# Kernel optimization log

Hardware: AMD Instinct MI355X
Metric: run time of the kernel (lower is better)

## Reference

```python
import jax, jax.numpy as jnp
import numpy as np
import math

B, S, HID, H, DH = 4, 1024, 1024, 16, 64  # batch, seq, hidden, heads, head_dim


def _rotate_half(x):
    x1, x2 = jnp.split(x, 2, axis=-1)
    return jnp.concatenate([-x2, x1], axis=-1)


def _apply_rope(t, freqs):
    # t: [B,H,S,DH], freqs: [S,rot_dim]; here rot_dim == DH so no pass-through part
    rot = freqs.shape[-1]
    cos_ = jnp.cos(freqs)[None, None, :, :].astype(t.dtype)
    sin_ = jnp.sin(freqs)[None, None, :, :].astype(t.dtype)
    t_rot, t_pass = t[..., :rot], t[..., rot:]
    t_rot = t_rot * cos_ + _rotate_half(t_rot) * sin_
    return jnp.concatenate([t_rot, t_pass], axis=-1)


def setup_inputs() -> dict:
    key = jax.random.key(0)
    ks = jax.random.split(key, 8)
    hidden_states = jax.random.normal(ks[0], (B, S, HID), dtype=jnp.float32)
    # additive mask: valid prefix of random length per batch row, -1e9 on padding
    lengths = jax.random.randint(ks[1], (B,), 3 * S // 4, S + 1)
    pos = jnp.arange(S)
    attention_mask = jnp.where(pos[None, :] < lengths[:, None], 0.0, -1e9)
    attention_mask = attention_mask.astype(jnp.float32)[:, None, None, :]  # [B,1,1,S]
    # rotary frequencies: standard RoPE angles, duplicated halves -> [S, DH]
    inv_freq = 1.0 / (10000.0 ** (jnp.arange(0, DH // 2, dtype=jnp.float32) / (DH // 2)))
    ang = pos.astype(jnp.float32)[:, None] * inv_freq[None, :]
    freqs = jnp.concatenate([ang, ang], axis=-1)  # [S, DH]
    sc = 0.02
    Wq = jax.random.normal(ks[2], (HID, HID), dtype=jnp.float32) * sc
    Wk = jax.random.normal(ks[3], (HID, HID), dtype=jnp.float32) * sc
    Wv = jax.random.normal(ks[4], (HID, HID), dtype=jnp.float32) * sc
    bq = jnp.zeros((HID,), dtype=jnp.float32)
    bk = jnp.zeros((HID,), dtype=jnp.float32)
    bv = jnp.zeros((HID,), dtype=jnp.float32)
    return dict(hidden_states=hidden_states, attention_mask=attention_mask, freqs=freqs,
                Wq=Wq, bq=bq, Wk=Wk, bk=bk, Wv=Wv, bv=bv)


def reference(hidden_states, attention_mask, freqs, Wq, bq, Wk, bk, Wv, bv):
    b, s, _ = hidden_states.shape
    # QKV projections -> [B,H,S,DH]
    q = (hidden_states @ Wq + bq).reshape(b, s, H, DH).transpose(0, 2, 1, 3)
    k = (hidden_states @ Wk + bk).reshape(b, s, H, DH).transpose(0, 2, 1, 3)
    v = (hidden_states @ Wv + bv).reshape(b, s, H, DH).transpose(0, 2, 1, 3)
    # inline RoPE on q and k (same freqs for both, as (rotary_pos_emb,)*2)
    q = _apply_rope(q, freqs)
    k = _apply_rope(k, freqs)
    scores = jnp.einsum('bhqd,bhkd->bhqk', q, k) / math.sqrt(DH)
    scores = scores + attention_mask  # additive mask broadcast over [B,H,S,S]
    probs = jax.nn.softmax(scores, axis=-1)
    # no_prob_mask filtering: zero out masked key columns
    probs = jnp.where(attention_mask < -1e-5, 0.0, probs)
    # dropout prob is 0.0 (eval) -> identity
    ctx = jnp.einsum('bhqk,bhkd->bhqd', probs, v)
    ctx = ctx.transpose(0, 2, 1, 3).reshape(b, s, H * DH)
    return ctx
```

## Files before the change

kernel.cpp:

```cpp
#include <hip/hip_runtime.h>
#include <hip/hip_bf16.h>
#include <cmath>

#define NB   4
#define NS   1024
#define NHID 1024
#define NH   16
#define NDH  64
#define QKV_PLANE (NB * NH * NS * NDH)

typedef __attribute__((ext_vector_type(8))) short bf16x8;
typedef __attribute__((ext_vector_type(4))) float f32x4;
typedef __attribute__((ext_vector_type(8))) unsigned short u16x8;

typedef __attribute__((address_space(1))) const void gv_t;
typedef __attribute__((address_space(3))) void       lv_t;

__device__ __forceinline__ void gload16(const void* g, void* l) {
    __builtin_amdgcn_global_load_lds((gv_t*)g, (lv_t*)l, 16, 0, 0);
}

__device__ __forceinline__ unsigned short f2b(float f) {
    union { float f; unsigned int u; } v; v.f = f;
    unsigned int r = (v.u + 0x7fff + ((v.u >> 16) & 1)) >> 16;
    return (unsigned short)r;
}

__device__ __forceinline__ unsigned int f2b2(float a, float b) {
    __hip_bfloat162 h = __float22bfloat162_rn(make_float2(a, b));
    union { __hip_bfloat162 h; unsigned int u; } v; v.h = h;
    return v.u;
}

__device__ __forceinline__ float fexp2(float x) {
#if __has_builtin(__builtin_amdgcn_exp2f)
    return __builtin_amdgcn_exp2f(x);
#else
    return exp2f(x);
#endif
}

__global__ __launch_bounds__(256) void prep_kernel(
    const float* __restrict__ hs, const float* __restrict__ freqs,
    const float* __restrict__ Wq, const float* __restrict__ Wk,
    const float* __restrict__ Wv,
    unsigned short* __restrict__ hsb, unsigned short* __restrict__ wt,
    float2* __restrict__ cs)
{
    const int z   = blockIdx.z;
    const int tid = threadIdx.x;

    if (z == 3) {
        const int bx = blockIdx.y * 16 + blockIdx.x;
        #pragma unroll
        for (int c = 0; c < 16; ++c) {
            const int idx = bx * 16384 + (c * 256 + tid) * 4;
            float4 v = *(const float4*)&hs[idx];
            ushort4 o;
            o.x = f2b(v.x); o.y = f2b(v.y); o.z = f2b(v.z); o.w = f2b(v.w);
            *(ushort4*)&hsb[idx] = o;
        }
        return;
    }
    if (z == 4) {
        const int bx = blockIdx.y * 16 + blockIdx.x;
        if (bx < 128) {
            const int id = bx * 256 + tid;
            const int s = id >> 5, d = id & 31;
            const float ang = freqs[s * NDH + d];
            float sn, cn;
            sincosf(ang, &sn, &cn);
            cs[id] = make_float2(cn, sn);
        }
        return;
    }

    const float* __restrict__ W = (z == 0) ? Wq : (z == 1) ? Wk : Wv;
    __shared__ float t[64][65];
    const int k0 = blockIdx.x * 64, n0 = blockIdx.y * 64;
    #pragma unroll
    for (int c = 0; c < 16; ++c) {
        const int flat = c * 256 + tid;
        const int r = flat >> 6, cc = flat & 63;
        t[r][cc] = W[(size_t)(k0 + r) * NHID + n0 + cc];
    }
    __syncthreads();
    #pragma unroll
    for (int c = 0; c < 16; ++c) {
        const int flat = c * 256 + tid;
        const int r = flat >> 6, cc = flat & 63;
        wt[(size_t)(z * 1024 + n0 + r) * NHID + k0 + cc] = f2b(t[cc][r]);
    }
}

__global__ __launch_bounds__(256) void fused_gemm_kernel(
    const unsigned short* __restrict__ hsb,
    const unsigned short* __restrict__ wt,
    const float2* __restrict__ cs,
    const float* __restrict__ bq, const float* __restrict__ bk,
    const float* __restrict__ bv,
    unsigned short* __restrict__ qkv)
{
    __shared__ short SH[16896];
    short* As = SH;
    short* Bs = SH + 8192;

    const int tid  = threadIdx.x;
    const int lane = tid & 63;
    const int wv   = __builtin_amdgcn_readfirstlane(tid >> 6);
    const bool vmode = (blockIdx.x >= 16);

    const unsigned short* Amat;
    const unsigned short* Bmat;
    int a_base, b_base, m0, n0, vb_ = 0;
    if (!vmode) {
        n0 = blockIdx.x * 128;
        m0 = blockIdx.y * 128;
        Amat = hsb;  a_base = m0;
        Bmat = wt;   b_base = n0;
    } else {
        m0  = (blockIdx.x - 16) * 128;
        vb_ = blockIdx.y >> 3;
        n0  = (blockIdx.y & 7) * 128;
        Amat = wt;   a_base = 2048 + m0;
        Bmat = hsb;  b_base = vb_ * 1024 + n0;
    }

    const int ri  = lane >> 3;
    const int kcs = ((lane & 7) ^ ri) * 8;
    const unsigned short* gA[4];
    const unsigned short* gB[4];
    short* lA[4];
    short* lB[4];
    #pragma unroll
    for (int j = 0; j < 4; ++j) {
        const int L = 4 * wv + j;
        gA[j] = Amat + (size_t)(a_base + L * 8 + ri) * NHID + kcs;
        gB[j] = Bmat + (size_t)(b_base + L * 8 + ri) * NHID + kcs;
        lA[j] = As + L * 512;
        lB[j] = Bs + L * 512;
    }

    const int R  = (wv & 1) * 64;
    const int CW = (wv >> 1) * 64;
    const int c0 = lane & 15;
    const int g  = lane >> 4;
    const int sw7 = c0 & 7;
    int aoff[4][2], boff[4][2];
    #pragma unroll
    for (int i = 0; i < 4; ++i)
        #pragma unroll
        for (int ks = 0; ks < 2; ++ks) {
            aoff[i][ks] = (R  + 16 * i + c0) * 64 + ((g + 4 * ks) ^ sw7) * 8;
            boff[i][ks] = (CW + 16 * i + c0) * 64 + ((g + 4 * ks) ^ sw7) * 8;
        }

    f32x4 acc[4][4] = {};

    for (int k0 = 0; k0 < NHID; k0 += 64) {
        __syncthreads();
        #pragma unroll
        for (int j = 0; j < 4; ++j) {
            gload16(gA[j] + k0, lA[j]);
            gload16(gB[j] + k0, lB[j]);
        }
        __syncthreads();
        #pragma unroll
        for (int ks = 0; ks < 2; ++ks) {
            bf16x8 af[4], bfr[4];
            #pragma unroll
            for (int i = 0; i < 4; ++i) af[i]  = *(const bf16x8*)&As[aoff[i][ks]];
            #pragma unroll
            for (int j = 0; j < 4; ++j) bfr[j] = *(const bf16x8*)&Bs[boff[j][ks]];
            #pragma unroll
            for (int i = 0; i < 4; ++i)
                #pragma unroll
                for (int j = 0; j < 4; ++j)
                    acc[i][j] = __builtin_amdgcn_mfma_f32_16x16x32_bf16(
                        af[i], bfr[j], acc[i][j], 0, 0, 0);
        }
    }

    __syncthreads();
    unsigned short* E = (unsigned short*)SH;
    const int qrow4 = (lane >> 4) * 4;

    if (!vmode) {
        const int z  = n0 >> 10;
        const int hd = ((n0 & 1023) + CW) >> 6;
        const float* __restrict__ bb = (z == 0) ? bq : bk;
        const float b0 = bb[hd * 64 + c0];
        const float b1 = bb[hd * 64 + c0 + 16];
        const float b2 = bb[hd * 64 + c0 + 32];
        const float b3 = bb[hd * 64 + c0 + 48];

        #pragma unroll
        for (int i = 0; i < 4; ++i) {
            #pragma unroll
            for (int r = 0; r < 4; ++r) {
                const int ml = R + qrow4 + 16 * i + r;
                const int s  = (m0 + ml) & 1023;
                float o0 = acc[i][0][r] + b0;
                float o1 = acc[i][1][r] + b1;
                float o2 = acc[i][2][r] + b2;
                float o3 = acc[i][3][r] + b3;
                const float2 cs0 = cs[s * 32 + c0];
                const float2 cs1 = cs[s * 32 + c0 + 16];
                unsigned short* e = E + ml * 132 + CW + c0;
                e[0]  = f2b(o0 * cs0.x - o2 * cs0.y);
                e[16] = f2b(o1 * cs1.x - o3 * cs1.y);
                e[32] = f2b(o2 * cs0.x + o0 * cs0.y);
                e[48] = f2b(o3 * cs1.x + o1 * cs1.y);
            }
        }
        __syncthreads();

        const int hd0 = (n0 & 1023) >> 6;
        unsigned short* __restrict__ base = qkv + (size_t)z * QKV_PLANE;
        #pragma unroll
        for (int c = 0; c < 8; ++c) {
            const int chunk = c * 256 + tid;
            const int row   = chunk >> 4;
            const int col16 = chunk & 15;
            const int m     = m0 + row;
            const int bidx  = m >> 10;
            const int s     = m & 1023;
            const int head  = hd0 + (col16 >> 3);
            const int d     = (col16 & 7) * 8;
            u16x8 v = *(const u16x8*)&E[row * 132 + col16 * 8];
            *(u16x8*)&base[(((size_t)bidx * NH + head) * NS + s) * NDH + d] = v;
        }
    } else {
        #pragma unroll
        for (int i = 0; i < 4; ++i) {
            #pragma unroll
            for (int r = 0; r < 4; ++r) {
                const int ml  = R + qrow4 + 16 * i + r;
                const float bvm = bv[m0 + ml];
                unsigned short* e = E + ml * 132 + CW + c0;
                e[0]  = f2b(acc[i][0][r] + bvm);
                e[16] = f2b(acc[i][1][r] + bvm);
                e[32] = f2b(acc[i][2][r] + bvm);
                e[48] = f2b(acc[i][3][r] + bvm);
            }
        }
        __syncthreads();

        unsigned short* __restrict__ vplane = qkv + 2 * (size_t)QKV_PLANE;
        #pragma unroll
        for (int c = 0; c < 8; ++c) {
            const int chunk = c * 256 + tid;
            const int row   = chunk >> 4;
            const int col16 = chunk & 15;
            u16x8 v = *(const u16x8*)&E[row * 132 + col16 * 8];
            *(u16x8*)&vplane[((size_t)(vb_ * 1024 + m0 + row)) * NS
                             + n0 + col16 * 8] = v;
        }
    }
}

__global__ __launch_bounds__(512) void attn_kernel(
    const unsigned short* __restrict__ qkv, const float* __restrict__ mask,
    float* __restrict__ out)
{
    const int qt = blockIdx.x, h = blockIdx.y, b = blockIdx.z;
    const unsigned short* qp  = qkv + ((size_t)(b * NH + h) * NS) * NDH;
    const unsigned short* kp  = qp + QKV_PLANE;
    const unsigned short* vtp = qkv + 2 * (size_t)QKV_PLANE
                              + ((size_t)(b * NH + h) * NDH) * NS;

    __shared__ unsigned short KsA[64 * 64];
    __shared__ unsigned short VtA[64 * 64];
    __shared__ unsigned short PsA[128 * 64];
    __shared__ float Mk[1024];
    __shared__ float Ll[128];

    const int tid  = threadIdx.x;
    const int lane = tid & 63;
    const int w    = __builtin_amdgcn_readfirstlane(tid >> 6);
    const int c0   = lane & 15;
    const int g    = lane >> 4;
    const int sw7  = c0 & 7;
    const float C1 = 0.125f * 1.44269504f;

    {
        const int i = tid * 2;
        float2 mv = *(const float2*)&mask[(size_t)b * NS + i];
        Mk[i]     = mv.x * 1.44269504f;
        Mk[i + 1] = mv.y * 1.44269504f;
    }

    bf16x8 qf[2];
    #pragma unroll
    for (int ks = 0; ks < 2; ++ks)
        qf[ks] = *(const bf16x8*)&qp[
            (size_t)(qt * 128 + w * 16 + c0) * NDH + g * 8 + ks * 32];

    const int i8 = lane >> 3, c8 = lane & 7;
    const int gsw = (c8 ^ i8) * 8;
    const unsigned short* gk = kp  + (size_t)(w * 8 + i8) * NDH + gsw;
    const unsigned short* gv = vtp + (size_t)(w * 8 + i8) * NS  + gsw;
    unsigned short* lk = KsA + w * 512;
    unsigned short* lv = VtA + w * 512;

    int kaddr[4][2], pw4[4], pr[2];
    #pragma unroll
    for (int mt = 0; mt < 4; ++mt)
        #pragma unroll
        for (int ks = 0; ks < 2; ++ks)
            kaddr[mt][ks] = (mt * 16 + c0) * 64 + ((g + ks * 4) ^ sw7) * 8;
    #pragma unroll
    for (int mt = 0; mt < 4; ++mt)
        pw4[mt] = (w * 16 + c0) * 64 + ((2 * mt + (g >> 1)) ^ sw7) * 8 + (g & 1) * 4;
    #pragma unroll
    for (int ks = 0; ks < 2; ++ks)
        pr[ks] = (w * 16 + c0) * 64 + ((g + ks * 4) ^ sw7) * 8;

    __syncthreads();
    int ktmax = 16;
    while (ktmax > 1 && Mk[(ktmax - 1) * 64] < -1.0f) --ktmax;

    float lrow = 0.f;
    f32x4 O[4] = {};

    for (int kt = 0; kt < ktmax; ++kt) {
        __syncthreads();
        gload16(gk, lk);
        gload16(gv, lv);
        gk += 64 * NDH;
        gv += 64;
        __syncthreads();

        bf16x8 kf[4][2];
        #pragma unroll
        for (int mt = 0; mt < 4; ++mt)
            #pragma unroll
            for (int ks = 0; ks < 2; ++ks)
                kf[mt][ks] = *(const bf16x8*)&KsA[kaddr[mt][ks]];
        f32x4 S[4];
        #pragma unroll
        for (int mt = 0; mt < 4; ++mt) {
            f32x4 a = {};
            a = __builtin_amdgcn_mfma_f32_16x16x32_bf16(kf[mt][0], qf[0], a, 0, 0, 0);
            a = __builtin_amdgcn_mfma_f32_16x16x32_bf16(kf[mt][1], qf[1], a, 0, 0, 0);
            S[mt] = a;
        }

        float psum = 0.f;
        #pragma unroll
        for (int mt = 0; mt < 4; ++mt) {
            float4 mv = *(const float4*)&Mk[kt * 64 + mt * 16 + g * 4];
            float p0 = fexp2(S[mt][0] * C1 + mv.x);
            float p1 = fexp2(S[mt][1] * C1 + mv.y);
            float p2 = fexp2(S[mt][2] * C1 + mv.z);
            float p3 = fexp2(S[mt][3] * C1 + mv.w);
            psum += (p0 + p1) + (p2 + p3);
            uint2 u;
            u.x = f2b2(p0, p1);
            u.y = f2b2(p2, p3);
            *(uint2*)&PsA[pw4[mt]] = u;
        }
        lrow += psum;

        bf16x8 pf[2], vf[4][2];
        #pragma unroll
        for (int ks = 0; ks < 2; ++ks)
            pf[ks] = *(const bf16x8*)&PsA[pr[ks]];
        #pragma unroll
        for (int nd = 0; nd < 4; ++nd)
            #pragma unroll
            for (int ks = 0; ks < 2; ++ks)
                vf[nd][ks] = *(const bf16x8*)&VtA[kaddr[nd][ks]];
        #pragma unroll
        for (int nd = 0; nd < 4; ++nd) {
            f32x4 o = O[nd];
            o = __builtin_amdgcn_mfma_f32_16x16x32_bf16(pf[0], vf[nd][0], o, 0, 0, 0);
            o = __builtin_amdgcn_mfma_f32_16x16x32_bf16(pf[1], vf[nd][1], o, 0, 0, 0);
            O[nd] = o;
        }
    }

    lrow += __shfl_xor(lrow, 16);
    lrow += __shfl_xor(lrow, 32);
    if (g == 0) Ll[w * 16 + c0] = lrow;
    float4 lv4 = *(const float4*)&Ll[w * 16 + g * 4];
    float inv[4];
    #pragma unroll
    for (int r = 0; r < 4; ++r) inv[r] = 1.0f / ((const float*)&lv4)[r];

    #pragma unroll
    for (int nd = 0; nd < 4; ++nd)
        #pragma unroll
        for (int r = 0; r < 4; ++r) {
            const int row = qt * 128 + w * 16 + g * 4 + r;
            const int col = h * 64 + nd * 16 + c0;
            out[((size_t)b * NS + row) * NHID + col] = O[nd][r] * inv[r];
        }
}

extern "C" void kernel_launch(void* const* d_in, const int* in_sizes, int n_in,
                              void* d_out, int out_size, void* d_ws, size_t ws_size,
                              hipStream_t stream) {
    const float* hs    = (const float*)d_in[0];
    const float* mask  = (const float*)d_in[1];
    const float* freqs = (const float*)d_in[2];
    const float* Wq    = (const float*)d_in[3];
    const float* bq    = (const float*)d_in[4];
    const float* Wk    = (const float*)d_in[5];
    const float* bk    = (const float*)d_in[6];
    const float* Wv    = (const float*)d_in[7];
    const float* bv    = (const float*)d_in[8];
    float* out = (float*)d_out;

    char* ws = (char*)d_ws;
    unsigned short* qkvb = (unsigned short*)ws;
    unsigned short* hsb  = (unsigned short*)(ws + 25165824);
    unsigned short* wtb  = (unsigned short*)(ws + 33554432);
    float2*         csb  = (float2*)       (ws + 39845888);

    prep_kernel<<<dim3(16, 16, 5), 256, 0, stream>>>(hs, freqs, Wq, Wk, Wv,
                                                     hsb, wtb, csb);
    fused_gemm_kernel<<<dim3(24, 32), 256, 0, stream>>>(hsb, wtb, csb,
                                                        bq, bk, bv, qkvb);
    attn_kernel<<<dim3(NS / 128, NH, NB), 512, 0, stream>>>(qkvb, mask, out);
}
```

Baseline: 155.7 us.

## Double-buffer K/V tiles in attention loop and raise MFMA wave priority

The attention kernel now keeps two LDS buffers for K and V^T. It prefetches the next 64-key tile with global_load_lds while the current tile is computed, which cuts the per-iteration barriers from two to one. The MFMA sections are wrapped in s_setprio to favour matrix issue across waves. LDS use grows by 16 KB per block, which may reduce occupancy. Correctness depends on the end-of-loop barrier waiting for the async LDS loads to finish.

```diff
diff --git a/kernel.cpp b/kernel.cpp
--- a/kernel.cpp
+++ b/kernel.cpp
@@ -269,8 +269,8 @@
     const unsigned short* vtp = qkv + 2 * (size_t)QKV_PLANE
                               + ((size_t)(b * NH + h) * NDH) * NS;
 
-    __shared__ unsigned short KsA[64 * 64];
-    __shared__ unsigned short VtA[64 * 64];
+    __shared__ unsigned short KsA[2][64 * 64];
+    __shared__ unsigned short VtA[2][64 * 64];
     __shared__ unsigned short PsA[128 * 64];
     __shared__ float Mk[1024];
     __shared__ float Ll[128];
@@ -298,10 +298,8 @@
 
     const int i8 = lane >> 3, c8 = lane & 7;
     const int gsw = (c8 ^ i8) * 8;
-    const unsigned short* gk = kp  + (size_t)(w * 8 + i8) * NDH + gsw;
-    const unsigned short* gv = vtp + (size_t)(w * 8 + i8) * NS  + gsw;
-    unsigned short* lk = KsA + w * 512;
-    unsigned short* lv = VtA + w * 512;
+    const unsigned short* gk0 = kp  + (size_t)(w * 8 + i8) * NDH + gsw;
+    const unsigned short* gv0 = vtp + (size_t)(w * 8 + i8) * NS  + gsw;
 
     int kaddr[4][2], pw4[4], pr[2];
     #pragma unroll
@@ -316,7 +314,10 @@
     for (int ks = 0; ks < 2; ++ks)
         pr[ks] = (w * 16 + c0) * 64 + ((g + ks * 4) ^ sw7) * 8;
 
+    gload16(gk0, &KsA[0][w * 512]);
+    gload16(gv0, &VtA[0][w * 512]);
     __syncthreads();
+
     int ktmax = 16;
     while (ktmax > 1 && Mk[(ktmax - 1) * 64] < -1.0f) --ktmax;
 
@@ -324,20 +325,24 @@
     f32x4 O[4] = {};
 
     for (int kt = 0; kt < ktmax; ++kt) {
-        __syncthreads();
-        gload16(gk, lk);
-        gload16(gv, lv);
-        gk += 64 * NDH;
-        gv += 64;
-        __syncthreads();
+        const int cur = kt & 1;
+
+        if (kt + 1 < ktmax) {
+            gload16(gk0 + (size_t)(kt + 1) * 64 * NDH, &KsA[cur ^ 1][w * 512]);
+            gload16(gv0 + (size_t)(kt + 1) * 64,       &VtA[cur ^ 1][w * 512]);
+        }
+
+        const unsigned short* Kb = KsA[cur];
+        const unsigned short* Vb = VtA[cur];
 
         bf16x8 kf[4][2];
         #pragma unroll
         for (int mt = 0; mt < 4; ++mt)
             #pragma unroll
             for (int ks = 0; ks < 2; ++ks)
-                kf[mt][ks] = *(const bf16x8*)&KsA[kaddr[mt][ks]];
+                kf[mt][ks] = *(const bf16x8*)&Kb[kaddr[mt][ks]];
         f32x4 S[4];
+        __builtin_amdgcn_s_setprio(1);
         #pragma unroll
         for (int mt = 0; mt < 4; ++mt) {
             f32x4 a = {};
@@ -345,6 +350,7 @@
             a = __builtin_amdgcn_mfma_f32_16x16x32_bf16(kf[mt][1], qf[1], a, 0, 0, 0);
             S[mt] = a;
         }
+        __builtin_amdgcn_s_setprio(0);
 
         float psum = 0.f;
         #pragma unroll
@@ -370,7 +376,8 @@
         for (int nd = 0; nd < 4; ++nd)
             #pragma unroll
             for (int ks = 0; ks < 2; ++ks)
-                vf[nd][ks] = *(const bf16x8*)&VtA[kaddr[nd][ks]];
+                vf[nd][ks] = *(const bf16x8*)&Vb[kaddr[nd][ks]];
+        __builtin_amdgcn_s_setprio(1);
         #pragma unroll
         for (int nd = 0; nd < 4; ++nd) {
             f32x4 o = O[nd];
@@ -378,6 +385,9 @@
             o = __builtin_amdgcn_mfma_f32_16x16x32_bf16(pf[1], vf[nd][1], o, 0, 0, 0);
             O[nd] = o;
         }
+        __builtin_amdgcn_s_setprio(0);
+
+        __syncthreads();
     }
 
     lrow += __shfl_xor(lrow, 16);
```

Result: no change. 155.6 us (-0.0%).
